# Performance work log

Measured on AMD Instinct MI355X. Metric: run time of the kernel, lower is better.

The kernel has to match this reference:

```python
import jax, jax.numpy as jnp
import numpy as np


def _rope_freqs(T, H, W, head_dim):
    # 3D RoPE frequency table, shape (T*H*W, head_dim)
    dim_t = head_dim - 4 * (head_dim // 6)
    dim_h = 2 * (head_dim // 6)
    dim_w = 2 * (head_dim // 6)
    base = 10000.0
    ft = 1.0 / base ** (np.arange(0, dim_t, 2)[: dim_t // 2].astype(np.float32) / dim_t)
    fh = 1.0 / base ** (np.arange(0, dim_h, 2)[: dim_h // 2].astype(np.float32) / dim_h)
    fw = 1.0 / base ** (np.arange(0, dim_w, 2)[: dim_w // 2].astype(np.float32) / dim_w)
    gt = np.arange(T, dtype=np.float32)
    gh = np.arange(H, dtype=np.float32)
    gw = np.arange(W, dtype=np.float32)
    # outer products, then repeat-interleave each freq twice: '... n -> ... (n r)', r=2
    Ft = np.repeat(gt[:, None] * ft[None, :], 2, axis=-1)  # [T, dim_t]
    Fh = np.repeat(gh[:, None] * fh[None, :], 2, axis=-1)  # [H, dim_h]
    Fw = np.repeat(gw[:, None] * fw[None, :], 2, axis=-1)  # [W, dim_w]
    Ft = np.broadcast_to(Ft[:, None, None, :], (T, H, W, Ft.shape[-1]))
    Fh = np.broadcast_to(Fh[None, :, None, :], (T, H, W, Fh.shape[-1]))
    Fw = np.broadcast_to(Fw[None, None, :, :], (T, H, W, Fw.shape[-1]))
    freqs = np.concatenate([Ft, Fh, Fw], axis=-1).reshape(T * H * W, head_dim)
    return jnp.asarray(freqs)


def _rotate_half(x):
    # pairs along last dim: (d r) with r=2 -> (-x2, x1)
    x = x.reshape(x.shape[:-1] + (x.shape[-1] // 2, 2))
    x1, x2 = x[..., 0], x[..., 1]
    return jnp.stack((-x2, x1), axis=-1).reshape(x.shape[:-2] + (-1,))


def _rms_norm(x, w, eps=1e-6):
    xf = x.astype(jnp.float32)
    y = xf * jax.lax.rsqrt(jnp.mean(xf * xf, axis=-1, keepdims=True) + eps)
    return y.astype(x.dtype) * w


def reference(x, qkv_w, qkv_b, q_norm_w, k_norm_w, proj_w, proj_b, t_size, h_size, w_size):
    B, N, C = x.shape
    Hn = 24
    D = C // Hn
    qkv = x @ qkv_w.T + qkv_b  # [B, N, 3C]
    qkv = qkv.reshape(B, N, 3, Hn, D).transpose(2, 0, 3, 1, 4)  # [3, B, H, N, D]
    q, k, v = qkv[0], qkv[1], qkv[2]
    q = _rms_norm(q, q_norm_w)
    k = _rms_norm(k, k_norm_w)
    # 3D RoPE
    freqs = _rope_freqs(int(t_size), int(h_size), int(w_size), D)  # [N, D]
    cos = jnp.cos(freqs)[None, None]  # [1,1,N,D]
    sin = jnp.sin(freqs)[None, None]
    qf, kf = q.astype(jnp.float32), k.astype(jnp.float32)
    q = (qf * cos + _rotate_half(qf) * sin).astype(q.dtype)
    k = (kf * cos + _rotate_half(kf) * sin).astype(k.dtype)
    # scaled dot-product attention
    scale = D ** -0.5
    scores = jnp.einsum('bhqd,bhkd->bhqk', q, k) * scale
    attn = jax.nn.softmax(scores, axis=-1)
    out = jnp.einsum('bhqk,bhkd->bhqd', attn, v)  # [B,H,N,D]
    out = out.transpose(0, 2, 1, 3).reshape(B, N, C)
    return out @ proj_w.T + proj_b


def setup_inputs() -> dict:
    key = jax.random.key(0)
    ks = jax.random.split(key, 6)
    B, N, C, D = 2, 2048, 3072, 128
    return {
        'x': jax.random.normal(ks[0], (B, N, C), jnp.float32),
        'qkv_w': jax.random.normal(ks[1], (3 * C, C), jnp.float32) * (C ** -0.5),
        'qkv_b': jax.random.normal(ks[2], (3 * C,), jnp.float32) * 0.02,
        'q_norm_w': jnp.ones((D,), jnp.float32),
        'k_norm_w': jnp.ones((D,), jnp.float32),
        'proj_w': jax.random.normal(ks[3], (C, C), jnp.float32) * (C ** -0.5),
        'proj_b': jax.random.normal(ks[4], (C,), jnp.float32) * 0.02,
        't_size': 8,
        'h_size': 16,
        'w_size': 16,
    }
```

## Files before the change

kernel.cpp:

```cpp
#include <hip/hip_runtime.h>
#include <math.h>

typedef __attribute__((ext_vector_type(8))) __bf16 bf16x8;
typedef __attribute__((ext_vector_type(4))) __bf16 bf16x4;
typedef __attribute__((ext_vector_type(2))) __bf16 bf16x2;
typedef __attribute__((ext_vector_type(4))) float f32x4;

#define MFMA16(a, b, c) __builtin_amdgcn_mfma_f32_16x16x32_bf16(a, b, c, 0, 0, 0)

typedef const __attribute__((address_space(1))) unsigned int* gas_t;
typedef __attribute__((address_space(3))) unsigned int* las_t;

__device__ __forceinline__ void g2lds16(const __bf16* g, __bf16* l) {
    __builtin_amdgcn_global_load_lds((gas_t)(const void*)g, (las_t)(void*)l, 16, 0, 0);
}

__global__ void pack_bf16(const float* __restrict__ src, __bf16* __restrict__ dst, int n4) {
    int idx = blockIdx.x * 256 + threadIdx.x;
    if (idx < n4) {
        float4 f = *(const float4*)(src + (size_t)idx * 4);
        bf16x4 o;
        o.x = (__bf16)f.x; o.y = (__bf16)f.y; o.z = (__bf16)f.z; o.w = (__bf16)f.w;
        *(bf16x4*)(dst + (size_t)idx * 4) = o;
    }
}

template <typename OutT>
__global__ void gemm_bt_bias(const __bf16* __restrict__ A, const __bf16* __restrict__ B,
                             const float* __restrict__ bias, OutT* __restrict__ C,
                             int M, int N, int K) {
    __shared__ __align__(16) __bf16 As[128 * 64];
    __shared__ __align__(16) __bf16 Bs[128 * 64];
    const int tid = threadIdx.x;
    const int lane = tid & 63, wave = tid >> 6;
    const int lm = lane & 15, q8 = (lane >> 4) * 8, quad = lane >> 4;
    const int wr = wave >> 1, wc = wave & 1;
    const int n0 = blockIdx.x * 128, m0 = blockIdx.y * 128;

    f32x4 acc[4][4] = {};

    for (int k0 = 0; k0 < K; k0 += 64) {
        __syncthreads();
        for (int it = 0; it < 4; ++it) {
            int c = it * 256 + tid;
            int row = c >> 3, ch = (c & 7) * 8;
            g2lds16(A + (size_t)(m0 + row) * K + k0 + ch, As + c * 8);
            g2lds16(B + (size_t)(n0 + row) * K + k0 + ch, Bs + c * 8);
        }
        __syncthreads();
        for (int kk = 0; kk < 64; kk += 32) {
            bf16x8 a[4], b[4];
            for (int i = 0; i < 4; ++i)
                a[i] = *(const bf16x8*)(As + (wr * 64 + i * 16 + lm) * 64 + kk + q8);
            for (int j = 0; j < 4; ++j)
                b[j] = *(const bf16x8*)(Bs + (wc * 64 + j * 16 + lm) * 64 + kk + q8);
            for (int i = 0; i < 4; ++i)
                for (int j = 0; j < 4; ++j)
                    acc[i][j] = MFMA16(a[i], b[j], acc[i][j]);
        }
    }
    for (int j = 0; j < 4; ++j) {
        int col = n0 + wc * 64 + j * 16 + lm;
        float bj = bias[col];
        for (int i = 0; i < 4; ++i) {
            int mb = m0 + wr * 64 + i * 16 + quad * 4;
            for (int r = 0; r < 4; ++r)
                C[(size_t)(mb + r) * N + col] = (OutT)(acc[i][j][r] + bj);
        }
    }
}

__global__ void rmsrope(__bf16* __restrict__ qkv, const float* __restrict__ qw,
                        const float* __restrict__ kw) {
    int bn = blockIdx.x;
    int n = bn & 2047;
    int tid = threadIdx.x, wave = tid >> 6, lane = tid & 63;
    int d0 = lane * 2;
    int t = n >> 8, hp = (n >> 4) & 15, wp = n & 15;
    float pos, fi;
    if (d0 < 44)      { pos = (float)t;  fi = (float)(d0 >> 1) * (2.0f / 44.0f); }
    else if (d0 < 86) { pos = (float)hp; fi = (float)((d0 - 44) >> 1) * (2.0f / 42.0f); }
    else              { pos = (float)wp; fi = (float)((d0 - 86) >> 1) * (2.0f / 42.0f); }
    float freq = expf(-fi * 9.210340371976184f);
    float ang = pos * freq, sn, cs;
    sincosf(ang, &sn, &cs);
    float w0q = qw[d0], w1q = qw[d0 + 1], w0k = kw[d0], w1k = kw[d0 + 1];

    for (int h = wave; h < 24; h += 4) {
        size_t base = (size_t)bn * 9216 + h * 128 + d0;
        {
            bf16x2 xv = *(bf16x2*)(qkv + base);
            float x0 = (float)xv.x, x1 = (float)xv.y;
            float ss = x0 * x0 + x1 * x1;
            for (int m = 1; m < 64; m <<= 1) ss += __shfl_xor(ss, m, 64);
            float rr = rsqrtf(ss * (1.0f / 128.0f) + 1e-6f);
            float y0 = x0 * rr * w0q, y1 = x1 * rr * w1q;
            bf16x2 st; st.x = (__bf16)(y0 * cs - y1 * sn); st.y = (__bf16)(y1 * cs + y0 * sn);
            *(bf16x2*)(qkv + base) = st;
        }
        {
            bf16x2 xv = *(bf16x2*)(qkv + base + 3072);
            float x0 = (float)xv.x, x1 = (float)xv.y;
            float ss = x0 * x0 + x1 * x1;
            for (int m = 1; m < 64; m <<= 1) ss += __shfl_xor(ss, m, 64);
            float rr = rsqrtf(ss * (1.0f / 128.0f) + 1e-6f);
            float y0 = x0 * rr * w0k, y1 = x1 * rr * w1k;
            bf16x2 st; st.x = (__bf16)(y0 * cs - y1 * sn); st.y = (__bf16)(y1 * cs + y0 * sn);
            *(bf16x2*)(qkv + base + 3072) = st;
        }
    }
}

__global__ __launch_bounds__(256, 2)
void flash(const __bf16* __restrict__ qkv, __bf16* __restrict__ Oo) {
    __shared__ __align__(16) __bf16 Ks[64 * 136];
    __shared__ __align__(16) __bf16 VTs[128 * 72];
    __shared__ __align__(16) __bf16 Ps[128 * 72];
    int bh = blockIdx.x >> 4, qt = blockIdx.x & 15;
    int b = bh / 24, h = bh % 24;
    int q0 = qt * 128;
    int tid = threadIdx.x, wave = tid >> 6, lane = tid & 63;
    int lm = lane & 15, q8 = (lane >> 4) * 8, quad = lane >> 4;
    int wb = wave * 32;
    const float sc = 0.08838834764831845f;

    bf16x8 qf[2][4];
    for (int i = 0; i < 2; ++i)
        for (int kk = 0; kk < 4; ++kk)
            qf[i][kk] = *(const bf16x8*)(qkv + (size_t)(b * 2048 + q0 + wb + i * 16 + lm) * 9216
                                         + h * 128 + kk * 32 + q8);

    float mrow[2] = {-__builtin_inff(), -__builtin_inff()};
    float lrow[2] = {0.f, 0.f};
    f32x4 oacc[2][8] = {};

    for (int nt = 0; nt < 32; ++nt) {
        int n0 = nt * 64;
        __syncthreads();
        for (int r = 0; r < 4; ++r) {
            int c = r * 256 + tid;
            int krow = c >> 4, kch = (c & 15) * 8;
            *(uint4*)(Ks + krow * 136 + kch) =
                *(const uint4*)(qkv + (size_t)(b * 2048 + n0 + krow) * 9216 + 3072 + h * 128 + kch);
            int vkey = c & 63, vch = (c >> 6) * 8;
            bf16x8 vv = *(const bf16x8*)(qkv + (size_t)(b * 2048 + n0 + vkey) * 9216 + 6144 + h * 128 + vch);
            for (int j = 0; j < 8; ++j)
                VTs[(vch + j) * 72 + vkey] = vv[j];
        }
        __syncthreads();

        f32x4 s[2][4] = {};
        for (int kk = 0; kk < 4; ++kk) {
            bf16x8 bk[4];
            for (int j = 0; j < 4; ++j)
                bk[j] = *(const bf16x8*)(Ks + (j * 16 + lm) * 136 + kk * 32 + q8);
            for (int i = 0; i < 2; ++i)
                for (int j = 0; j < 4; ++j)
                    s[i][j] = MFMA16(bk[j], qf[i][kk], s[i][j]);
        }
        for (int i = 0; i < 2; ++i) {
            float mx = -__builtin_inff();
            for (int j = 0; j < 4; ++j)
                for (int r = 0; r < 4; ++r)
                    mx = fmaxf(mx, s[i][j][r]);
            mx *= sc;
            mx = fmaxf(mx, __shfl_xor(mx, 16, 64));
            mx = fmaxf(mx, __shfl_xor(mx, 32, 64));
            float mn = fmaxf(mrow[i], mx);
            float alpha = __expf(mrow[i] - mn);
            mrow[i] = mn;
            float rs = 0.f;
            for (int j = 0; j < 4; ++j) {
                bf16x4 pw;
                for (int r = 0; r < 4; ++r) {
                    float p = __expf(s[i][j][r] * sc - mn);
                    rs += p;
                    pw[r] = (__bf16)p;
                }
                *(bf16x4*)(Ps + (wb + i * 16 + lm) * 72 + j * 16 + quad * 4) = pw;
            }
            rs += __shfl_xor(rs, 16, 64);
            rs += __shfl_xor(rs, 32, 64);
            lrow[i] = lrow[i] * alpha + rs;
            if (__any(alpha != 1.0f))
                for (int ct = 0; ct < 8; ++ct) oacc[i][ct] *= alpha;
        }
        for (int kk = 0; kk < 2; ++kk) {
            bf16x8 ap[2];
            for (int i = 0; i < 2; ++i)
                ap[i] = *(const bf16x8*)(Ps + (wb + i * 16 + lm) * 72 + kk * 32 + q8);
            for (int ct = 0; ct < 8; ++ct) {
                bf16x8 bv = *(const bf16x8*)(VTs + (ct * 16 + lm) * 72 + kk * 32 + q8);
                for (int i = 0; i < 2; ++i)
                    oacc[i][ct] = MFMA16(bv, ap[i], oacc[i][ct]);
            }
        }
    }
    for (int i = 0; i < 2; ++i) {
        float inv = 1.0f / lrow[i];
        int row = q0 + wb + i * 16 + lm;
        size_t base = ((size_t)b * 2048 + row) * 3072 + h * 128 + quad * 4;
        for (int ct = 0; ct < 8; ++ct) {
            bf16x4 ov;
            for (int r = 0; r < 4; ++r) ov[r] = (__bf16)(oacc[i][ct][r] * inv);
            *(bf16x4*)(Oo + base + ct * 16) = ov;
        }
    }
}

extern "C" void kernel_launch(void* const* d_in, const int* in_sizes, int n_in,
                              void* d_out, int out_size, void* d_ws, size_t ws_size,
                              hipStream_t stream) {
    const float* x      = (const float*)d_in[0];
    const float* qkv_w  = (const float*)d_in[1];
    const float* qkv_b  = (const float*)d_in[2];
    const float* qnw    = (const float*)d_in[3];
    const float* knw    = (const float*)d_in[4];
    const float* proj_w = (const float*)d_in[5];
    const float* proj_b = (const float*)d_in[6];
    float* out = (float*)d_out;
    char* ws = (char*)d_ws;

    __bf16* xb   = (__bf16*)(ws + 0);
    __bf16* attn = (__bf16*)(ws + 0);
    __bf16* w1b  = (__bf16*)(ws + 25165824);
    __bf16* w2b  = (__bf16*)(ws + 81788928);
    __bf16* qkvb = (__bf16*)(ws + 100663296);

    pack_bf16<<<12288, 256, 0, stream>>>(x, xb, 3145728);
    pack_bf16<<<27648, 256, 0, stream>>>(qkv_w, w1b, 7077888);
    pack_bf16<<<9216, 256, 0, stream>>>(proj_w, w2b, 2359296);

    gemm_bt_bias<__bf16><<<dim3(72, 32), 256, 0, stream>>>(xb, w1b, qkv_b, qkvb, 4096, 9216, 3072);

    rmsrope<<<4096, 256, 0, stream>>>(qkvb, qnw, knw);

    flash<<<768, 256, 0, stream>>>(qkvb, attn);

    gemm_bt_bias<float><<<dim3(24, 32), 256, 0, stream>>>(attn, w2b, proj_b, out, 4096, 3072, 3072);
}
```

Baseline: 789.1 us.

## Replace GEMM with 256x256 double-buffered, swizzled, pipelined MFMA kernel

Both projection GEMMs move from a 128x128 tile kernel with 256 threads and a single LDS buffer to a 256x256 tile kernel with 512 threads. The new kernel double-buffers LDS and interleaves half-tile global-to-LDS loads with MFMA quarters under manual waitcnt and barrier control. It also XOR-swizzles LDS columns to avoid bank conflicts and remaps workgroups in groups of eight to improve L2 locality. The aim is to hide load latency and raise arithmetic intensity, at the cost of heavy register pressure and fragile hand-written synchronization.

Result: slower. 823.2 us (+4.3%).

```diff
diff --git a/kernel.cpp b/kernel.cpp
--- a/kernel.cpp
+++ b/kernel.cpp
@@ -25,47 +25,122 @@
     }
 }
 
+
+#define STAGE_A(bufi, hh, tt) do {                                                     \
+    _Pragma("unroll")                                                                  \
+    for (int l = 0; l < 2; ++l) {                                                      \
+        int c = (l << 9) + tid, rh = c >> 3;                                           \
+        int esw = ((c & 7) << 3) ^ ((rh & 7) << 3);                                    \
+        int gm = m0 + ((rh >> 6) << 7) + ((hh) << 6) + (rh & 63);                      \
+        g2lds16(A + (size_t)gm * K + ((tt) << 6) + esw, &As[bufi][hh][c << 3]);        \
+    } } while (0)
+
+#define STAGE_B(bufi, hh, tt) do {                                                     \
+    _Pragma("unroll")                                                                  \
+    for (int l = 0; l < 2; ++l) {                                                      \
+        int c = (l << 9) + tid, rh = c >> 3;                                           \
+        int esw = ((c & 7) << 3) ^ ((rh & 7) << 3);                                    \
+        int gn = n0 + ((rh >> 5) << 6) + ((hh) << 5) + (rh & 31);                      \
+        g2lds16(B + (size_t)gn * K + ((tt) << 6) + esw, &Bs[bufi][hh][c << 3]);        \
+    } } while (0)
+
+#define READ_A(bufi, hh) do {                                                          \
+    _Pragma("unroll")                                                                  \
+    for (int m2 = 0; m2 < 4; ++m2) {                                                   \
+        _Pragma("unroll")                                                              \
+        for (int kk = 0; kk < 2; ++kk)                                                 \
+            af[m2][kk] = *(const bf16x8*)&As[bufi][hh][                                \
+                (((wm << 6) + (m2 << 4) + lm) << 6) + (((kk << 5) + q8) ^ swz)];       \
+    } } while (0)
+
+#define READ_B(dst, bufi, hh) do {                                                     \
+    _Pragma("unroll")                                                                  \
+    for (int n2 = 0; n2 < 2; ++n2) {                                                   \
+        _Pragma("unroll")                                                              \
+        for (int kk = 0; kk < 2; ++kk)                                                 \
+            dst[n2][kk] = *(const bf16x8*)&Bs[bufi][hh][                               \
+                (((wn << 5) + (n2 << 4) + lm) << 6) + (((kk << 5) + q8) ^ swz)];       \
+    } } while (0)
+
+#define MMA_Q(mh, bvar, nh) do {                                                       \
+    __builtin_amdgcn_s_setprio(1);                                                     \
+    _Pragma("unroll")                                                                  \
+    for (int m2 = 0; m2 < 4; ++m2) {                                                   \
+        _Pragma("unroll")                                                              \
+        for (int n2 = 0; n2 < 2; ++n2) {                                               \
+            _Pragma("unroll")                                                          \
+            for (int kk = 0; kk < 2; ++kk)                                             \
+                acc[(mh) * 4 + m2][(nh) * 2 + n2] =                                    \
+                    MFMA16(af[m2][kk], bvar[n2][kk], acc[(mh) * 4 + m2][(nh) * 2 + n2]); \
+    } }                                                                                \
+    __builtin_amdgcn_s_setprio(0); } while (0)
+
+#define BAR __builtin_amdgcn_s_barrier()
+#define MID do { BAR; asm volatile("s_waitcnt lgkmcnt(0)" ::: "memory"); } while (0)
+#define VMW(n) asm volatile("s_waitcnt vmcnt(" #n ")" ::: "memory")
+#define NOPS ((void)0)
+
+#define TILE4(bufi, S1, S2, S3, S4, W4) do {                                           \
+    READ_A(bufi, 0); READ_B(be, bufi, 0);                                              \
+    S1; MID; MMA_Q(0, be, 0); BAR;                                                     \
+    READ_B(bo, bufi, 1);                                                               \
+    S2; MID; MMA_Q(0, bo, 1); BAR;                                                     \
+    READ_A(bufi, 1);                                                                   \
+    S3; MID; MMA_Q(1, bo, 1); BAR;                                                     \
+    S4; W4; BAR; MMA_Q(1, be, 0); BAR; } while (0)
+
 template <typename OutT>
-__global__ void gemm_bt_bias(const __bf16* __restrict__ A, const __bf16* __restrict__ B,
-                             const float* __restrict__ bias, OutT* __restrict__ C,
-                             int M, int N, int K) {
-    __shared__ __align__(16) __bf16 As[128 * 64];
-    __shared__ __align__(16) __bf16 Bs[128 * 64];
+__global__ __launch_bounds__(512, 2)
+void gemm256_bt_bias(const __bf16* __restrict__ A, const __bf16* __restrict__ B,
+                     const float* __restrict__ bias, OutT* __restrict__ C,
+                     int M, int N, int K) {
+    __shared__ __align__(16) __bf16 As[2][2][8192];
+    __shared__ __align__(16) __bf16 Bs[2][2][8192];
+
     const int tid = threadIdx.x;
     const int lane = tid & 63, wave = tid >> 6;
-    const int lm = lane & 15, q8 = (lane >> 4) * 8, quad = lane >> 4;
-    const int wr = wave >> 1, wc = wave & 1;
-    const int n0 = blockIdx.x * 128, m0 = blockIdx.y * 128;
-
-    f32x4 acc[4][4] = {};
-
-    for (int k0 = 0; k0 < K; k0 += 64) {
-        __syncthreads();
-        for (int it = 0; it < 4; ++it) {
-            int c = it * 256 + tid;
-            int row = c >> 3, ch = (c & 7) * 8;
-            g2lds16(A + (size_t)(m0 + row) * K + k0 + ch, As + c * 8);
-            g2lds16(B + (size_t)(n0 + row) * K + k0 + ch, Bs + c * 8);
-        }
-        __syncthreads();
-        for (int kk = 0; kk < 64; kk += 32) {
-            bf16x8 a[4], b[4];
-            for (int i = 0; i < 4; ++i)
-                a[i] = *(const bf16x8*)(As + (wr * 64 + i * 16 + lm) * 64 + kk + q8);
-            for (int j = 0; j < 4; ++j)
-                b[j] = *(const bf16x8*)(Bs + (wc * 64 + j * 16 + lm) * 64 + kk + q8);
-            for (int i = 0; i < 4; ++i)
-                for (int j = 0; j < 4; ++j)
-                    acc[i][j] = MFMA16(a[i], b[j], acc[i][j]);
-        }
-    }
-    for (int j = 0; j < 4; ++j) {
-        int col = n0 + wc * 64 + j * 16 + lm;
-        float bj = bias[col];
-        for (int i = 0; i < 4; ++i) {
-            int mb = m0 + wr * 64 + i * 16 + quad * 4;
+    const int lm = lane & 15, quad = lane >> 4, q8 = quad << 3;
+    const int wm = wave >> 2, wn = wave & 3;
+    const int swz = (lm & 7) << 3;
+
+    const int nwg = gridDim.x;
+    const int wg = (blockIdx.x & 7) * (nwg >> 3) + (blockIdx.x >> 3);
+    const int nbx = N >> 8;
+    const int m0 = (wg / nbx) << 8;
+    const int n0 = (wg % nbx) << 8;
+
+    const int NT = K >> 6, ITER = NT >> 1;
+
+    f32x4 acc[8][4] = {};
+    bf16x8 af[4][2], be[2][2], bo[2][2];
+
+    STAGE_A(0, 0, 0); STAGE_B(0, 0, 0); STAGE_B(0, 1, 0); STAGE_A(0, 1, 0);
+    STAGE_A(1, 0, 1); STAGE_B(1, 0, 1); STAGE_B(1, 1, 1);
+    VMW(6);
+    BAR;
+
+#pragma unroll 1
+    for (int i = 0; i < ITER - 1; ++i) {
+        const int b = 2 * i + 1, t2 = 2 * i + 2, t3 = 2 * i + 3;
+        TILE4(0, STAGE_A(1, 1, b),  STAGE_A(0, 0, t2), STAGE_B(0, 0, t2), STAGE_B(0, 1, t2), VMW(6));
+        TILE4(1, STAGE_A(0, 1, t2), STAGE_A(1, 0, t3), STAGE_B(1, 0, t3), STAGE_B(1, 1, t3), VMW(6));
+    }
+    {
+        const int b = NT - 1;
+        TILE4(0, STAGE_A(1, 1, b), NOPS, NOPS, NOPS, VMW(0));
+        TILE4(1, NOPS, NOPS, NOPS, NOPS, NOPS);
+    }
+
+#pragma unroll
+    for (int nf = 0; nf < 4; ++nf) {
+        const int col = n0 + (wn << 6) + (nf << 4) + lm;
+        const float bj = bias[col];
+#pragma unroll
+        for (int mf = 0; mf < 8; ++mf) {
+            const int mb = m0 + (wm << 7) + (mf << 4) + (quad << 2);
+#pragma unroll
             for (int r = 0; r < 4; ++r)
-                C[(size_t)(mb + r) * N + col] = (OutT)(acc[i][j][r] + bj);
+                C[(size_t)(mb + r) * N + col] = (OutT)(acc[mf][nf][r] + bj);
         }
     }
 }
@@ -231,11 +306,11 @@
     pack_bf16<<<27648, 256, 0, stream>>>(qkv_w, w1b, 7077888);
     pack_bf16<<<9216, 256, 0, stream>>>(proj_w, w2b, 2359296);
 
-    gemm_bt_bias<__bf16><<<dim3(72, 32), 256, 0, stream>>>(xb, w1b, qkv_b, qkvb, 4096, 9216, 3072);
+    gemm256_bt_bias<__bf16><<<576, 512, 0, stream>>>(xb, w1b, qkv_b, qkvb, 4096, 9216, 3072);
 
     rmsrope<<<4096, 256, 0, stream>>>(qkvb, qnw, knw);
 
     flash<<<768, 256, 0, stream>>>(qkvb, attn);
 
-    gemm_bt_bias<float><<<dim3(24, 32), 256, 0, stream>>>(attn, w2b, proj_b, out, 4096, 3072, 3072);
-}
+    gemm256_bt_bias<float><<<192, 512, 0, stream>>>(attn, w2b, proj_b, out, 4096, 3072, 3072);
+}
```
